# Performance work log

Hardware: AMD Instinct MI355X
Metric: run time of the kernel (lower is better)

Reference implementation:

```python
import jax, jax.numpy as jnp
import numpy as np

D_MODEL = 2048
N_Q_HEADS = 32
N_KV_HEADS = 8
HEAD_DIM = D_MODEL // N_Q_HEADS  # 64
KV_DIM = HEAD_DIM * N_KV_HEADS   # 512
B, S = 2, 2048


def setup_inputs() -> dict:
    key = jax.random.key(0)
    ks = jax.random.split(key, 11)
    sc_d = 1.0 / np.sqrt(D_MODEL)
    return {
        "query": jax.random.normal(ks[0], (B, S, D_MODEL), jnp.float32),
        "key":   jax.random.normal(ks[1], (B, S, D_MODEL), jnp.float32),
        "value": jax.random.normal(ks[2], (B, S, D_MODEL), jnp.float32),
        "Wq": jax.random.normal(ks[3], (D_MODEL, D_MODEL), jnp.float32) * sc_d,
        "bq": jnp.zeros((D_MODEL,), jnp.float32),
        "Wk": jax.random.normal(ks[4], (D_MODEL, KV_DIM), jnp.float32) * sc_d,
        "bk": jnp.zeros((KV_DIM,), jnp.float32),
        "Wv": jax.random.normal(ks[5], (D_MODEL, KV_DIM), jnp.float32) * sc_d,
        "bv": jnp.zeros((KV_DIM,), jnp.float32),
        "Wo": jax.random.normal(ks[6], (D_MODEL, D_MODEL), jnp.float32) * sc_d,
        "bo": jnp.zeros((D_MODEL,), jnp.float32),
    }


def reference(query, key, value, Wq, bq, Wk, bk, Wv, bv, Wo, bo):
    b, s, _ = query.shape
    g = N_Q_HEADS // N_KV_HEADS  # num groups
    # projections
    Q = query @ Wq + bq                      # [b, s, d_model]
    K = key @ Wk + bk                        # [b, s, kv_dim]
    V = value @ Wv + bv                      # [b, s, kv_dim]
    # split heads. Torch code splits Q into groups of num_kv_heads heads,
    # and each group broadcasts per-head against the Hkv KV heads, i.e.
    # query head (grp*Hkv + j) attends against kv head j.
    Q = Q.reshape(b, s, g, N_KV_HEADS, HEAD_DIM)  # [b, s, g, hkv, d]
    K = K.reshape(b, s, N_KV_HEADS, HEAD_DIM)     # [b, s, hkv, d]
    V = V.reshape(b, s, N_KV_HEADS, HEAD_DIM)
    scale = 1.0 / jnp.sqrt(jnp.float32(HEAD_DIM))
    scores = jnp.einsum('bsghd,bthd->bghst', Q, K) * scale  # [b,g,hkv,s,s]
    attn = jax.nn.softmax(scores, axis=-1)
    out = jnp.einsum('bghst,bthd->bsghd', attn, V)          # [b,s,g,hkv,d]
    # concat over groups then heads == original head order (g major, hkv minor)
    out = out.reshape(b, s, D_MODEL)
    return out @ Wo + bo
```

## Files before the change

kernel.cpp:

```cpp
#include <hip/hip_runtime.h>
#include <cstdint>

typedef _Float16 half4 __attribute__((ext_vector_type(4)));
typedef _Float16 half8 __attribute__((ext_vector_type(8)));
typedef _Float16 half16 __attribute__((ext_vector_type(16)));
typedef float f32x4 __attribute__((ext_vector_type(4)));
typedef float f32x16 __attribute__((ext_vector_type(16)));

#define L2E 1.44269504088896340736f

__device__ __forceinline__ void gl16(const void* g, void* l) {
  __builtin_amdgcn_global_load_lds(
      (const __attribute__((address_space(1))) void*)g,
      (__attribute__((address_space(3))) void*)l, 16, 0, 0);
}

__device__ __forceinline__ uint32_t pk2(float a, float b) {
  return __builtin_bit_cast(uint32_t, __builtin_amdgcn_cvt_pkrtz(a, b));
}

__device__ __forceinline__ void plswap(uint32_t& x, uint32_t& y) {
  auto r = __builtin_amdgcn_permlane32_swap((int)x, (int)y, false, false);
  x = (uint32_t)r[0];
  y = (uint32_t)r[1];
}

__device__ __forceinline__ f32x16 zero16() {
  f32x16 z;
  #pragma unroll
  for (int r = 0; r < 16; ++r) z[r] = 0.0f;
  return z;
}

__global__ __launch_bounds__(256) void cvt_f32_f16_3(
    const float* __restrict__ s0, const float* __restrict__ s1, const float* __restrict__ s2,
    _Float16* __restrict__ d0, _Float16* __restrict__ d1, _Float16* __restrict__ d2)
{
  const float* src = (blockIdx.z == 0) ? s0 : (blockIdx.z == 1 ? s1 : s2);
  _Float16* dst    = (blockIdx.z == 0) ? d0 : (blockIdx.z == 1 ? d1 : d2);
  size_t i = ((size_t)blockIdx.x * 256 + threadIdx.x) * 8;
  float4 a = *(const float4*)(src + i);
  float4 b = *(const float4*)(src + i + 4);
  half8 o;
  o[0] = (_Float16)a.x; o[1] = (_Float16)a.y; o[2] = (_Float16)a.z; o[3] = (_Float16)a.w;
  o[4] = (_Float16)b.x; o[5] = (_Float16)b.y; o[6] = (_Float16)b.z; o[7] = (_Float16)b.w;
  *(half8*)(dst + i) = o;
}

__global__ __launch_bounds__(256) void transpose_w_all(
    const float* __restrict__ Wq, const float* __restrict__ Wk,
    const float* __restrict__ Wv, const float* __restrict__ Wo,
    _Float16* __restrict__ WqkvT, _Float16* __restrict__ WoT)
{
  int id = blockIdx.x;
  const float* src;
  _Float16* dst;
  int N, tx, ty;
  if (id < 4096)      { src = Wq; dst = WqkvT;                        N = 2048; tx = id & 63; ty = id >> 6; }
  else if (id < 5120) { id -= 4096; src = Wk; dst = WqkvT + (size_t)2048 * 2048; N = 512; tx = id & 15; ty = id >> 4; }
  else if (id < 6144) { id -= 5120; src = Wv; dst = WqkvT + (size_t)2560 * 2048; N = 512; tx = id & 15; ty = id >> 4; }
  else                { id -= 6144; src = Wo; dst = WoT;              N = 2048; tx = id & 63; ty = id >> 6; }
  const int n0 = tx * 32, k0 = ty * 32;
  __shared__ float t[32][33];
  #pragma unroll
  for (int i = 0; i < 4; ++i)
    t[threadIdx.y + i * 8][threadIdx.x] =
        src[(size_t)(k0 + threadIdx.y + i * 8) * N + n0 + threadIdx.x];
  __syncthreads();
  #pragma unroll
  for (int i = 0; i < 4; ++i)
    dst[(size_t)(n0 + threadIdx.y + i * 8) * 2048 + k0 + threadIdx.x] =
        (_Float16)t[threadIdx.x][threadIdx.y + i * 8];
}

__global__ __launch_bounds__(256) void transpose_v(
    const _Float16* __restrict__ QKV, _Float16* __restrict__ VT)
{
  const int bh = blockIdx.z;
  const int bb = bh >> 3, h = bh & 7;
  const int t0 = blockIdx.x * 32, d0 = blockIdx.y * 32;
  __shared__ _Float16 t[32][33];
  const _Float16* src = QKV + (size_t)(bb * 2048) * 3072 + 2560 + h * 64;
  #pragma unroll
  for (int i = 0; i < 4; ++i)
    t[threadIdx.y + i * 8][threadIdx.x] =
        src[(size_t)(t0 + threadIdx.y + i * 8) * 3072 + d0 + threadIdx.x];
  __syncthreads();
  _Float16* dst = VT + ((size_t)(bb * 8 + h) * 64) * 2048;
  #pragma unroll
  for (int i = 0; i < 4; ++i)
    dst[(size_t)(d0 + threadIdx.y + i * 8) * 2048 + t0 + threadIdx.x] =
        t[threadIdx.x][threadIdx.y + i * 8];
}

template<int MODE>
__global__ __launch_bounds__(512, 2) void gemm128(
    const _Float16* __restrict__ Aq, const _Float16* __restrict__ Ak, const _Float16* __restrict__ Av,
    const _Float16* __restrict__ Bt,
    const float* __restrict__ bias0, const float* __restrict__ bias1, const float* __restrict__ bias2,
    _Float16* __restrict__ Ch, float* __restrict__ Cf)
{
  constexpr int K = 2048;
  constexpr int N = (MODE == 0) ? 3072 : 2048;
  constexpr int NB = N / 256;
  constexpr int G = 32 * NB;
  constexpr int BUF = 8192 + 16384;

  const int wg = blockIdx.x;
  const int work = (wg & 7) * (G / 8) + (wg >> 3);
  const int m0 = (work / NB) * 128;
  const int n0 = (work % NB) * 256;

  const _Float16* A = Aq;
  if constexpr (MODE == 0) { if (n0 >= 2560) A = Av; else if (n0 >= 2048) A = Ak; }

  const int tid = threadIdx.x;
  const int lane = tid & 63;
  const int w = tid >> 6;
  const int wr = w >> 2;
  const int wc = w & 3;
  const int lo = lane & 15, hi = lane >> 4;

  __shared__ __align__(1024) char smem[3 * BUF];

  f32x4 acc[4][4];
  #pragma unroll
  for (int mt = 0; mt < 4; ++mt)
    #pragma unroll
    for (int nt = 0; nt < 4; ++nt)
      acc[mt][nt] = (f32x4){0.f, 0.f, 0.f, 0.f};

  const _Float16* pB = Bt + (size_t)(n0 + w * 32 + (lane >> 2)) * K + (lane & 3) * 8;
  const _Float16* pA = A  + (size_t)(m0 + w * 16 + (lane >> 2)) * K + (lane & 3) * 8;
  const size_t bstep = (size_t)16 * K;
  const int dstB = 8192 + w * 2048;
  const int dstA = w * 1024;

  gl16(pA,      smem + dstA);
  gl16(pB,      smem + dstB);        gl16(pB + bstep,      smem + dstB + 1024);
  gl16(pA + 32, smem + BUF + dstA);
  gl16(pB + 32, smem + BUF + dstB);  gl16(pB + 32 + bstep, smem + BUF + dstB + 1024);
  pA += 64; pB += 64;
  asm volatile("s_waitcnt vmcnt(3)" ::: "memory");
  __builtin_amdgcn_s_barrier();

  const int abase = (wr * 64 + lo) * 64 + hi * 16;
  const int bbase = 8192 + (wc * 64 + lo) * 64 + hi * 16;

  int c = 0;
  for (int t = 0; t < 64; ++t) {
    int c1 = c + 1; if (c1 == 3) c1 = 0;
    int c2 = c1 + 1; if (c2 == 3) c2 = 0;
    if (t < 62) {
      char* bp_ = smem + c2 * BUF;
      gl16(pA, bp_ + dstA);
      gl16(pB, bp_ + dstB);
      gl16(pB + bstep, bp_ + dstB + 1024);
      pA += 32; pB += 32;
    }

    const char* bc = smem + c * BUF;
    half8 af[4], bf[4];
    #pragma unroll
    for (int mt = 0; mt < 4; ++mt) af[mt] = *(const half8*)(bc + abase + mt * 1024);
    #pragma unroll
    for (int nt = 0; nt < 4; ++nt) bf[nt] = *(const half8*)(bc + bbase + nt * 1024);

    __builtin_amdgcn_s_setprio(1);
    #pragma unroll
    for (int mt = 0; mt < 4; ++mt)
      #pragma unroll
      for (int nt = 0; nt < 4; ++nt)
        acc[mt][nt] = __builtin_amdgcn_mfma_f32_16x16x32_f16(af[mt], bf[nt], acc[mt][nt], 0, 0, 0);
    __builtin_amdgcn_s_setprio(0);

    if (t < 62)       asm volatile("s_waitcnt vmcnt(3)" ::: "memory");
    else if (t == 62) asm volatile("s_waitcnt vmcnt(0)" ::: "memory");
    if (t < 63) __builtin_amdgcn_s_barrier();
    c = c1;
  }

  float* T = (float*)smem;
  const int tr = tid >> 4;
  const int sc = tid & 15;
  #pragma unroll
  for (int mp = 0; mp < 4; ++mp) {
    __syncthreads();
    #pragma unroll
    for (int nt = 0; nt < 4; ++nt)
      #pragma unroll
      for (int r = 0; r < 4; ++r)
        T[(wr * 16 + 4 * hi + r) * 256 + wc * 64 + nt * 16 + lo] = acc[mp][nt][r];
    __syncthreads();
    const int grow = m0 + (tr >> 4) * 64 + mp * 16 + (tr & 15);
    const int gcol = n0 + sc * 16;
    const float* Trow = T + tr * 256 + sc * 16;
    float4 v[4];
    #pragma unroll
    for (int q = 0; q < 4; ++q) v[q] = ((const float4*)Trow)[q];
    const float* bp = bias0;
    int cb = gcol;
    if constexpr (MODE == 0) {
      if (gcol >= 2560) { bp = bias2; cb = gcol - 2560; }
      else if (gcol >= 2048) { bp = bias1; cb = gcol - 2048; }
    }
    float4 bvv[4];
    #pragma unroll
    for (int q = 0; q < 4; ++q) bvv[q] = ((const float4*)(bp + cb))[q];
    if constexpr (MODE == 0) {
      half16 o;
      #pragma unroll
      for (int q = 0; q < 4; ++q) {
        o[4 * q + 0] = (_Float16)(v[q].x + bvv[q].x);
        o[4 * q + 1] = (_Float16)(v[q].y + bvv[q].y);
        o[4 * q + 2] = (_Float16)(v[q].z + bvv[q].z);
        o[4 * q + 3] = (_Float16)(v[q].w + bvv[q].w);
      }
      *(half16*)(Ch + (size_t)grow * N + gcol) = o;
    } else {
      float* dstp = Cf + (size_t)grow * N + gcol;
      #pragma unroll
      for (int q = 0; q < 4; ++q) {
        float4 ov = {v[q].x + bvv[q].x, v[q].y + bvv[q].y, v[q].z + bvv[q].z, v[q].w + bvv[q].w};
        ((float4*)dstp)[q] = ov;
      }
    }
  }
}

__global__ __launch_bounds__(256, 5) void attn_fwd4(
    const _Float16* __restrict__ QKV, const _Float16* __restrict__ VT,
    _Float16* __restrict__ AO)
{
  const int wg = blockIdx.x;
  const int work = (wg & 7) * 128 + (wg >> 3);
  const int bh = work >> 6;
  const int b = bh >> 3, h = bh & 7;
  const int rem = work & 63;
  const int qh = (rem >> 4) * 8 + h;
  const int qt = rem & 15;

  const int tid = threadIdx.x;
  const int lane = tid & 63;
  const int w = tid >> 6;
  const int l31 = lane & 31;
  const int hi5 = lane >> 5;
  const int r7 = l31 & 7;

  __shared__ __align__(1024) char sm[2][2][8192];

  const _Float16 QSC = (_Float16)(0.125f * L2E);
  const int qrow0 = b * 2048 + qt * 128 + w * 32 + l31;
  half8 qf[4];
  {
    const _Float16* qp = QKV + (size_t)qrow0 * 3072 + qh * 64 + hi5 * 8;
    #pragma unroll
    for (int s = 0; s < 4; ++s) {
      half8 q = *(const half8*)(qp + s * 16);
      #pragma unroll
      for (int e = 0; e < 8; ++e) q[e] = q[e] * QSC;
      qf[s] = q;
    }
  }

  const int li = lane >> 3;
  const int lc = lane & 7;
  const int kslot = lc ^ li;
  const int w16li = w * 16 + li;
  const _Float16* Ksrc = QKV + ((size_t)(b * 2048 + w16li)) * 3072 + 2048 + h * 64 + kslot * 8;
  const _Float16* Vsrc = VT + ((size_t)(b * 8 + h) * 64 + w16li) * 2048 + kslot * 8;

  f32x16 oa[2];
  oa[0] = zero16();
  oa[1] = zero16();
  float lreg = 0.f;

  {
    char* kd = &sm[0][0][0] + w * 2048;
    char* vd = &sm[0][1][0] + w * 2048;
    gl16(Ksrc, kd);
    gl16(Ksrc + (size_t)8 * 3072, kd + 1024);
    gl16(Vsrc, vd);
    gl16(Vsrc + (size_t)8 * 2048, vd + 1024);
  }
  __syncthreads();

  int cur = 0;
  for (int t = 0; t < 32; ++t) {
    if (t < 31) {
      const int t0 = (t + 1) * 64;
      char* kd = &sm[cur ^ 1][0][0] + w * 2048;
      char* vd = &sm[cur ^ 1][1][0] + w * 2048;
      const _Float16* kg = Ksrc + (size_t)t0 * 3072;
      const _Float16* vg = Vsrc + t0;
      gl16(kg, kd);
      gl16(kg + (size_t)8 * 3072, kd + 1024);
      gl16(vg, vd);
      gl16(vg + (size_t)8 * 2048, vd + 1024);
    }

    const char* Kb = &sm[cur][0][0];
    const char* Vb = &sm[cur][1][0];

    uint32_t pw[4][4];
    float ps = 0.f;
    #pragma unroll
    for (int j = 0; j < 2; ++j) {
      f32x16 sa = zero16();
      const int kr = j * 32 + l31;
      __builtin_amdgcn_s_setprio(1);
      #pragma unroll
      for (int s = 0; s < 4; ++s) {
        half8 kf = *(const half8*)(Kb + kr * 128 + (((2 * s + hi5) ^ r7) << 4));
        sa = __builtin_amdgcn_mfma_f32_32x32x16_f16(kf, qf[s], sa, 0, 0, 0);
      }
      __builtin_amdgcn_s_setprio(0);
      #pragma unroll
      for (int r = 0; r < 16; ++r) {
        const float p = __builtin_amdgcn_exp2f(sa[r]);
        sa[r] = p;
        ps += p;
      }
      #pragma unroll
      for (int hf = 0; hf < 2; ++hf) {
        const int rb = hf * 8;
        uint32_t w0 = pk2(sa[rb + 0], sa[rb + 1]);
        uint32_t w1 = pk2(sa[rb + 2], sa[rb + 3]);
        uint32_t w2 = pk2(sa[rb + 4], sa[rb + 5]);
        uint32_t w3 = pk2(sa[rb + 6], sa[rb + 7]);
        plswap(w0, w2);
        plswap(w1, w3);
        const int s = 2 * j + hf;
        pw[s][0] = w0; pw[s][1] = w1; pw[s][2] = w2; pw[s][3] = w3;
      }
    }
    ps += __shfl_xor(ps, 32);
    lreg += ps;

    __builtin_amdgcn_s_setprio(1);
    #pragma unroll
    for (int s = 0; s < 4; ++s) {
      union { uint32_t u[4]; half8 h; } p0;
      #pragma unroll
      for (int u = 0; u < 4; ++u) p0.u[u] = pw[s][u];
      #pragma unroll
      for (int i = 0; i < 2; ++i) {
        const int vr = i * 32 + l31;
        half8 vf = *(const half8*)(Vb + vr * 128 + (((2 * s + hi5) ^ r7) << 4));
        oa[i] = __builtin_amdgcn_mfma_f32_32x32x16_f16(vf, p0.h, oa[i], 0, 0, 0);
      }
    }
    __builtin_amdgcn_s_setprio(0);

    __syncthreads();
    cur ^= 1;
  }

  {
    const float inv = 1.0f / lreg;
    #pragma unroll
    for (int i = 0; i < 2; ++i) {
      _Float16* dst = AO + (size_t)qrow0 * 2048 + qh * 64 + i * 32 + hi5 * 4;
      #pragma unroll
      for (int q = 0; q < 4; ++q) {
        union { uint32_t u[2]; half4 h4; } o;
        o.u[0] = pk2(oa[i][4 * q + 0] * inv, oa[i][4 * q + 1] * inv);
        o.u[1] = pk2(oa[i][4 * q + 2] * inv, oa[i][4 * q + 3] * inv);
        *(half4*)(dst + 8 * q) = o.h4;
      }
    }
  }
}

extern "C" void kernel_launch(void* const* d_in, const int* in_sizes, int n_in,
                              void* d_out, int out_size, void* d_ws, size_t ws_size,
                              hipStream_t stream) {
  const float* query = (const float*)d_in[0];
  const float* key   = (const float*)d_in[1];
  const float* value = (const float*)d_in[2];
  const float* Wq = (const float*)d_in[3];
  const float* bq = (const float*)d_in[4];
  const float* Wk = (const float*)d_in[5];
  const float* bk = (const float*)d_in[6];
  const float* Wv = (const float*)d_in[7];
  const float* bv = (const float*)d_in[8];
  const float* Wo = (const float*)d_in[9];
  const float* bo = (const float*)d_in[10];
  float* out = (float*)d_out;

  char* ws = (char*)d_ws;
  _Float16* qh    = (_Float16*)(ws);
  _Float16* kh    = (_Float16*)(ws + 16777216);
  _Float16* vh    = (_Float16*)(ws + 33554432);
  _Float16* WqkvT = (_Float16*)(ws + 50331648);
  _Float16* WoT   = (_Float16*)(ws + 62914560);
  _Float16* QKVh  = (_Float16*)(ws + 71303168);
  _Float16* VT    = (_Float16*)(ws + 96468992);
  _Float16* aoh   = (_Float16*)(ws + 100663296);

  cvt_f32_f16_3<<<dim3(4096, 1, 3), 256, 0, stream>>>(query, key, value, qh, kh, vh);
  transpose_w_all<<<10240, dim3(32, 8), 0, stream>>>(Wq, Wk, Wv, Wo, WqkvT, WoT);
  gemm128<0><<<384, 512, 0, stream>>>(qh, kh, vh, WqkvT, bq, bk, bv, QKVh, nullptr);
  transpose_v<<<dim3(64, 2, 16), dim3(32, 8), 0, stream>>>(QKVh, VT);
  attn_fwd4<<<1024, 256, 0, stream>>>(QKVh, VT, aoh);
  gemm128<1><<<256, 512, 0, stream>>>(aoh, nullptr, nullptr, WoT, bo,
                                      nullptr, nullptr, nullptr, out);
}
```

Measured before the change: 248.2 us.

## Triple-buffer attention K/V loads and merge prep kernels into one launch

The attention kernel moves from double to triple buffering of K/V tiles in LDS. It prefetches two tiles ahead and replaces the full __syncthreads with an explicit vmcnt wait plus barrier, so global loads overlap more compute. The occupancy hint drops from 5 to 3 blocks per CU to fit the larger LDS footprint. Separately, the f32-to-f16 input conversion and the weight transposes are fused into a single prep kernel launch, removing one launch.

Result: no change. 244.0 us (-1.7%).

```diff
diff --git a/kernel.cpp b/kernel.cpp
--- a/kernel.cpp
+++ b/kernel.cpp
@@ -32,27 +32,30 @@
   return z;
 }
 
-__global__ __launch_bounds__(256) void cvt_f32_f16_3(
-    const float* __restrict__ s0, const float* __restrict__ s1, const float* __restrict__ s2,
-    _Float16* __restrict__ d0, _Float16* __restrict__ d1, _Float16* __restrict__ d2)
-{
-  const float* src = (blockIdx.z == 0) ? s0 : (blockIdx.z == 1 ? s1 : s2);
-  _Float16* dst    = (blockIdx.z == 0) ? d0 : (blockIdx.z == 1 ? d1 : d2);
-  size_t i = ((size_t)blockIdx.x * 256 + threadIdx.x) * 8;
-  float4 a = *(const float4*)(src + i);
-  float4 b = *(const float4*)(src + i + 4);
-  half8 o;
-  o[0] = (_Float16)a.x; o[1] = (_Float16)a.y; o[2] = (_Float16)a.z; o[3] = (_Float16)a.w;
-  o[4] = (_Float16)b.x; o[5] = (_Float16)b.y; o[6] = (_Float16)b.z; o[7] = (_Float16)b.w;
-  *(half8*)(dst + i) = o;
-}
-
-__global__ __launch_bounds__(256) void transpose_w_all(
+__global__ __launch_bounds__(256) void prep_all(
+    const float* __restrict__ q, const float* __restrict__ k, const float* __restrict__ v,
     const float* __restrict__ Wq, const float* __restrict__ Wk,
     const float* __restrict__ Wv, const float* __restrict__ Wo,
+    _Float16* __restrict__ qh, _Float16* __restrict__ kh, _Float16* __restrict__ vh,
     _Float16* __restrict__ WqkvT, _Float16* __restrict__ WoT)
 {
   int id = blockIdx.x;
+  const int tid = threadIdx.y * 32 + threadIdx.x;
+  if (id < 12288) {
+    const int z = id >> 12;
+    const int x = id & 4095;
+    const float* src = (z == 0) ? q : (z == 1 ? k : v);
+    _Float16* dst    = (z == 0) ? qh : (z == 1 ? kh : vh);
+    size_t i = ((size_t)x * 256 + tid) * 8;
+    float4 a = *(const float4*)(src + i);
+    float4 b = *(const float4*)(src + i + 4);
+    half8 o;
+    o[0] = (_Float16)a.x; o[1] = (_Float16)a.y; o[2] = (_Float16)a.z; o[3] = (_Float16)a.w;
+    o[4] = (_Float16)b.x; o[5] = (_Float16)b.y; o[6] = (_Float16)b.z; o[7] = (_Float16)b.w;
+    *(half8*)(dst + i) = o;
+    return;
+  }
+  id -= 12288;
   const float* src;
   _Float16* dst;
   int N, tx, ty;
@@ -197,7 +200,7 @@
     const float* Trow = T + tr * 256 + sc * 16;
     float4 v[4];
     #pragma unroll
-    for (int q = 0; q < 4; ++q) v[q] = ((const float4*)Trow)[q];
+    for (int qq = 0; qq < 4; ++qq) v[qq] = ((const float4*)Trow)[qq];
     const float* bp = bias0;
     int cb = gcol;
     if constexpr (MODE == 0) {
@@ -206,29 +209,29 @@
     }
     float4 bvv[4];
     #pragma unroll
-    for (int q = 0; q < 4; ++q) bvv[q] = ((const float4*)(bp + cb))[q];
+    for (int qq = 0; qq < 4; ++qq) bvv[qq] = ((const float4*)(bp + cb))[qq];
     if constexpr (MODE == 0) {
       half16 o;
       #pragma unroll
-      for (int q = 0; q < 4; ++q) {
-        o[4 * q + 0] = (_Float16)(v[q].x + bvv[q].x);
-        o[4 * q + 1] = (_Float16)(v[q].y + bvv[q].y);
-        o[4 * q + 2] = (_Float16)(v[q].z + bvv[q].z);
-        o[4 * q + 3] = (_Float16)(v[q].w + bvv[q].w);
+      for (int qq = 0; qq < 4; ++qq) {
+        o[4 * qq + 0] = (_Float16)(v[qq].x + bvv[qq].x);
+        o[4 * qq + 1] = (_Float16)(v[qq].y + bvv[qq].y);
+        o[4 * qq + 2] = (_Float16)(v[qq].z + bvv[qq].z);
+        o[4 * qq + 3] = (_Float16)(v[qq].w + bvv[qq].w);
       }
       *(half16*)(Ch + (size_t)grow * N + gcol) = o;
     } else {
       float* dstp = Cf + (size_t)grow * N + gcol;
       #pragma unroll
-      for (int q = 0; q < 4; ++q) {
-        float4 ov = {v[q].x + bvv[q].x, v[q].y + bvv[q].y, v[q].z + bvv[q].z, v[q].w + bvv[q].w};
-        ((float4*)dstp)[q] = ov;
-      }
-    }
-  }
-}
-
-__global__ __launch_bounds__(256, 5) void attn_fwd4(
+      for (int qq = 0; qq < 4; ++qq) {
+        float4 ov = {v[qq].x + bvv[qq].x, v[qq].y + bvv[qq].y, v[qq].z + bvv[qq].z, v[qq].w + bvv[qq].w};
+        ((float4*)dstp)[qq] = ov;
+      }
+    }
+  }
+}
+
+__global__ __launch_bounds__(256, 3) void attn_fwd5(
     const _Float16* __restrict__ QKV, const _Float16* __restrict__ VT,
     _Float16* __restrict__ AO)
 {
@@ -247,7 +250,7 @@
   const int hi5 = lane >> 5;
   const int r7 = l31 & 7;
 
-  __shared__ __align__(1024) char sm[2][2][8192];
+  __shared__ __align__(1024) char sm[3][2][8192];
 
   const _Float16 QSC = (_Float16)(0.125f * L2E);
   const int qrow0 = b * 2048 + qt * 128 + w * 32 + l31;
@@ -275,29 +278,28 @@
   oa[1] = zero16();
   float lreg = 0.f;
 
-  {
-    char* kd = &sm[0][0][0] + w * 2048;
-    char* vd = &sm[0][1][0] + w * 2048;
-    gl16(Ksrc, kd);
-    gl16(Ksrc + (size_t)8 * 3072, kd + 1024);
-    gl16(Vsrc, vd);
-    gl16(Vsrc + (size_t)8 * 2048, vd + 1024);
-  }
-  __syncthreads();
+  #define STAGE_KV(buf, tile)                                                 \
+    do {                                                                      \
+      char* kd_ = &sm[(buf)][0][0] + w * 2048;                                \
+      char* vd_ = &sm[(buf)][1][0] + w * 2048;                                \
+      const _Float16* kg_ = Ksrc + (size_t)(tile) * 64 * 3072;                \
+      const _Float16* vg_ = Vsrc + (tile) * 64;                               \
+      gl16(kg_, kd_);                                                         \
+      gl16(kg_ + (size_t)8 * 3072, kd_ + 1024);                               \
+      gl16(vg_, vd_);                                                         \
+      gl16(vg_ + (size_t)8 * 2048, vd_ + 1024);                               \
+    } while (0)
+
+  STAGE_KV(0, 0);
+  STAGE_KV(1, 1);
+  asm volatile("s_waitcnt vmcnt(4)" ::: "memory");
+  __builtin_amdgcn_s_barrier();
 
   int cur = 0;
   for (int t = 0; t < 32; ++t) {
-    if (t < 31) {
-      const int t0 = (t + 1) * 64;
-      char* kd = &sm[cur ^ 1][0][0] + w * 2048;
-      char* vd = &sm[cur ^ 1][1][0] + w * 2048;
-      const _Float16* kg = Ksrc + (size_t)t0 * 3072;
-      const _Float16* vg = Vsrc + t0;
-      gl16(kg, kd);
-      gl16(kg + (size_t)8 * 3072, kd + 1024);
-      gl16(vg, vd);
-      gl16(vg + (size_t)8 * 2048, vd + 1024);
-    }
+    int c1 = cur + 1; if (c1 == 3) c1 = 0;
+    int c2 = c1 + 1; if (c2 == 3) c2 = 0;
+    if (t < 30) STAGE_KV(c2, t + 2);
 
     const char* Kb = &sm[cur][0][0];
     const char* Vb = &sm[cur][1][0];
@@ -352,9 +354,12 @@
     }
     __builtin_amdgcn_s_setprio(0);
 
-    __syncthreads();
-    cur ^= 1;
-  }
+    if (t < 30)       asm volatile("s_waitcnt vmcnt(4)" ::: "memory");
+    else if (t == 30) asm volatile("s_waitcnt vmcnt(0)" ::: "memory");
+    if (t < 31) __builtin_amdgcn_s_barrier();
+    cur = c1;
+  }
+  #undef STAGE_KV
 
   {
     const float inv = 1.0f / lreg;
@@ -398,11 +403,11 @@
   _Float16* VT    = (_Float16*)(ws + 96468992);
   _Float16* aoh   = (_Float16*)(ws + 100663296);
 
-  cvt_f32_f16_3<<<dim3(4096, 1, 3), 256, 0, stream>>>(query, key, value, qh, kh, vh);
-  transpose_w_all<<<10240, dim3(32, 8), 0, stream>>>(Wq, Wk, Wv, Wo, WqkvT, WoT);
+  prep_all<<<22528, dim3(32, 8), 0, stream>>>(query, key, value, Wq, Wk, Wv, Wo,
+                                              qh, kh, vh, WqkvT, WoT);
   gemm128<0><<<384, 512, 0, stream>>>(qh, kh, vh, WqkvT, bq, bk, bv, QKVh, nullptr);
   transpose_v<<<dim3(64, 2, 16), dim3(32, 8), 0, stream>>>(QKVh, VT);
-  attn_fwd4<<<1024, 256, 0, stream>>>(QKVh, VT, aoh);
+  attn_fwd5<<<1024, 256, 0, stream>>>(QKVh, VT, aoh);
   gemm128<1><<<256, 512, 0, stream>>>(aoh, nullptr, nullptr, WoT, bo,
                                       nullptr, nullptr, nullptr, out);
 }
```

## Merge prep kernels, halve QKV GEMM tile width, adjust attention occupancy

Applied to the files above, without the earlier changes.

Fuses the input f32->f16 conversion and the weight transpose kernels into one launch. The QKV projection GEMM now uses 128-wide N tiles instead of 256, which doubles the workgroup count from 384 to 768 so more CUs stay busy, at the cost of less B-operand reuse per tile. The attention kernel's launch bounds drop its occupancy hint from 5 to 4 waves, which may give it more registers per thread.

Result: faster. 239.2 us (-3.6%).

```diff
diff --git a/kernel.cpp b/kernel.cpp
--- a/kernel.cpp
+++ b/kernel.cpp
@@ -32,27 +32,30 @@
   return z;
 }
 
-__global__ __launch_bounds__(256) void cvt_f32_f16_3(
-    const float* __restrict__ s0, const float* __restrict__ s1, const float* __restrict__ s2,
-    _Float16* __restrict__ d0, _Float16* __restrict__ d1, _Float16* __restrict__ d2)
-{
-  const float* src = (blockIdx.z == 0) ? s0 : (blockIdx.z == 1 ? s1 : s2);
-  _Float16* dst    = (blockIdx.z == 0) ? d0 : (blockIdx.z == 1 ? d1 : d2);
-  size_t i = ((size_t)blockIdx.x * 256 + threadIdx.x) * 8;
-  float4 a = *(const float4*)(src + i);
-  float4 b = *(const float4*)(src + i + 4);
-  half8 o;
-  o[0] = (_Float16)a.x; o[1] = (_Float16)a.y; o[2] = (_Float16)a.z; o[3] = (_Float16)a.w;
-  o[4] = (_Float16)b.x; o[5] = (_Float16)b.y; o[6] = (_Float16)b.z; o[7] = (_Float16)b.w;
-  *(half8*)(dst + i) = o;
-}
-
-__global__ __launch_bounds__(256) void transpose_w_all(
+__global__ __launch_bounds__(256) void prep_all(
+    const float* __restrict__ q, const float* __restrict__ k, const float* __restrict__ v,
     const float* __restrict__ Wq, const float* __restrict__ Wk,
     const float* __restrict__ Wv, const float* __restrict__ Wo,
+    _Float16* __restrict__ qh, _Float16* __restrict__ kh, _Float16* __restrict__ vh,
     _Float16* __restrict__ WqkvT, _Float16* __restrict__ WoT)
 {
   int id = blockIdx.x;
+  const int tid = threadIdx.y * 32 + threadIdx.x;
+  if (id < 12288) {
+    const int z = id >> 12;
+    const int x = id & 4095;
+    const float* src = (z == 0) ? q : (z == 1 ? k : v);
+    _Float16* dst    = (z == 0) ? qh : (z == 1 ? kh : vh);
+    size_t i = ((size_t)x * 256 + tid) * 8;
+    float4 a = *(const float4*)(src + i);
+    float4 b = *(const float4*)(src + i + 4);
+    half8 o;
+    o[0] = (_Float16)a.x; o[1] = (_Float16)a.y; o[2] = (_Float16)a.z; o[3] = (_Float16)a.w;
+    o[4] = (_Float16)b.x; o[5] = (_Float16)b.y; o[6] = (_Float16)b.z; o[7] = (_Float16)b.w;
+    *(half8*)(dst + i) = o;
+    return;
+  }
+  id -= 12288;
   const float* src;
   _Float16* dst;
   int N, tx, ty;
@@ -102,14 +105,18 @@
 {
   constexpr int K = 2048;
   constexpr int N = (MODE == 0) ? 3072 : 2048;
-  constexpr int NB = N / 256;
+  constexpr int BN = (MODE == 0) ? 128 : 256;
+  constexpr int NB = N / BN;
   constexpr int G = 32 * NB;
-  constexpr int BUF = 8192 + 16384;
+  constexpr int BUFB = BN * 64;
+  constexpr int BUF = 8192 + BUFB;
+  constexpr int NT = BN / 64;
+  constexpr int NVM = 1 + BN / 128;
 
   const int wg = blockIdx.x;
   const int work = (wg & 7) * (G / 8) + (wg >> 3);
   const int m0 = (work / NB) * 128;
-  const int n0 = (work % NB) * 256;
+  const int n0 = (work % NB) * BN;
 
   const _Float16* A = Aq;
   if constexpr (MODE == 0) { if (n0 >= 2560) A = Av; else if (n0 >= 2048) A = Ak; }
@@ -123,112 +130,118 @@
 
   __shared__ __align__(1024) char smem[3 * BUF];
 
-  f32x4 acc[4][4];
+  f32x4 acc[4][NT];
   #pragma unroll
   for (int mt = 0; mt < 4; ++mt)
     #pragma unroll
-    for (int nt = 0; nt < 4; ++nt)
+    for (int nt = 0; nt < NT; ++nt)
       acc[mt][nt] = (f32x4){0.f, 0.f, 0.f, 0.f};
 
-  const _Float16* pB = Bt + (size_t)(n0 + w * 32 + (lane >> 2)) * K + (lane & 3) * 8;
+  const _Float16* pB = Bt + (size_t)(n0 + w * (BN / 8) + (lane >> 2)) * K + (lane & 3) * 8;
   const _Float16* pA = A  + (size_t)(m0 + w * 16 + (lane >> 2)) * K + (lane & 3) * 8;
   const size_t bstep = (size_t)16 * K;
-  const int dstB = 8192 + w * 2048;
+  const int dstB = 8192 + w * (BN / 8) * 64;
   const int dstA = w * 1024;
 
-  gl16(pA,      smem + dstA);
-  gl16(pB,      smem + dstB);        gl16(pB + bstep,      smem + dstB + 1024);
-  gl16(pA + 32, smem + BUF + dstA);
-  gl16(pB + 32, smem + BUF + dstB);  gl16(pB + 32 + bstep, smem + BUF + dstB + 1024);
-  pA += 64; pB += 64;
-  asm volatile("s_waitcnt vmcnt(3)" ::: "memory");
+  #define STAGE(base)                                                         \
+    do {                                                                      \
+      gl16(pA, (base) + dstA);                                                \
+      gl16(pB, (base) + dstB);                                                \
+      if constexpr (MODE == 1) gl16(pB + bstep, (base) + dstB + 1024);        \
+    } while (0)
+
+  STAGE(smem);
+  pA += 32; pB += 32;
+  STAGE(smem + BUF);
+  pA += 32; pB += 32;
+  asm volatile("s_waitcnt vmcnt(%0)" :: "i"(NVM) : "memory");
   __builtin_amdgcn_s_barrier();
 
   const int abase = (wr * 64 + lo) * 64 + hi * 16;
-  const int bbase = 8192 + (wc * 64 + lo) * 64 + hi * 16;
+  const int bbase = 8192 + (wc * (BN / 4) + lo) * 64 + hi * 16;
 
   int c = 0;
   for (int t = 0; t < 64; ++t) {
     int c1 = c + 1; if (c1 == 3) c1 = 0;
     int c2 = c1 + 1; if (c2 == 3) c2 = 0;
     if (t < 62) {
-      char* bp_ = smem + c2 * BUF;
-      gl16(pA, bp_ + dstA);
-      gl16(pB, bp_ + dstB);
-      gl16(pB + bstep, bp_ + dstB + 1024);
+      STAGE(smem + c2 * BUF);
       pA += 32; pB += 32;
     }
 
     const char* bc = smem + c * BUF;
-    half8 af[4], bf[4];
+    half8 af[4], bf[NT];
     #pragma unroll
     for (int mt = 0; mt < 4; ++mt) af[mt] = *(const half8*)(bc + abase + mt * 1024);
     #pragma unroll
-    for (int nt = 0; nt < 4; ++nt) bf[nt] = *(const half8*)(bc + bbase + nt * 1024);
+    for (int nt = 0; nt < NT; ++nt) bf[nt] = *(const half8*)(bc + bbase + nt * 1024);
 
     __builtin_amdgcn_s_setprio(1);
     #pragma unroll
     for (int mt = 0; mt < 4; ++mt)
       #pragma unroll
-      for (int nt = 0; nt < 4; ++nt)
+      for (int nt = 0; nt < NT; ++nt)
         acc[mt][nt] = __builtin_amdgcn_mfma_f32_16x16x32_f16(af[mt], bf[nt], acc[mt][nt], 0, 0, 0);
     __builtin_amdgcn_s_setprio(0);
 
-    if (t < 62)       asm volatile("s_waitcnt vmcnt(3)" ::: "memory");
+    if (t < 62)       asm volatile("s_waitcnt vmcnt(%0)" :: "i"(NVM) : "memory");
     else if (t == 62) asm volatile("s_waitcnt vmcnt(0)" ::: "memory");
     if (t < 63) __builtin_amdgcn_s_barrier();
     c = c1;
   }
+  #undef STAGE
 
   float* T = (float*)smem;
   const int tr = tid >> 4;
   const int sc = tid & 15;
+  constexpr int CPS = BN / 16;
   #pragma unroll
   for (int mp = 0; mp < 4; ++mp) {
     __syncthreads();
     #pragma unroll
-    for (int nt = 0; nt < 4; ++nt)
+    for (int nt = 0; nt < NT; ++nt)
       #pragma unroll
       for (int r = 0; r < 4; ++r)
-        T[(wr * 16 + 4 * hi + r) * 256 + wc * 64 + nt * 16 + lo] = acc[mp][nt][r];
+        T[(wr * 16 + 4 * hi + r) * BN + wc * (BN / 4) + nt * 16 + lo] = acc[mp][nt][r];
     __syncthreads();
     const int grow = m0 + (tr >> 4) * 64 + mp * 16 + (tr & 15);
-    const int gcol = n0 + sc * 16;
-    const float* Trow = T + tr * 256 + sc * 16;
-    float4 v[4];
-    #pragma unroll
-    for (int q = 0; q < 4; ++q) v[q] = ((const float4*)Trow)[q];
+    const int gcol = n0 + sc * CPS;
+    const float* Trow = T + tr * BN + sc * CPS;
     const float* bp = bias0;
     int cb = gcol;
     if constexpr (MODE == 0) {
       if (gcol >= 2560) { bp = bias2; cb = gcol - 2560; }
       else if (gcol >= 2048) { bp = bias1; cb = gcol - 2048; }
     }
-    float4 bvv[4];
-    #pragma unroll
-    for (int q = 0; q < 4; ++q) bvv[q] = ((const float4*)(bp + cb))[q];
     if constexpr (MODE == 0) {
-      half16 o;
-      #pragma unroll
-      for (int q = 0; q < 4; ++q) {
-        o[4 * q + 0] = (_Float16)(v[q].x + bvv[q].x);
-        o[4 * q + 1] = (_Float16)(v[q].y + bvv[q].y);
-        o[4 * q + 2] = (_Float16)(v[q].z + bvv[q].z);
-        o[4 * q + 3] = (_Float16)(v[q].w + bvv[q].w);
-      }
-      *(half16*)(Ch + (size_t)grow * N + gcol) = o;
+      float4 v0 = ((const float4*)Trow)[0];
+      float4 v1 = ((const float4*)Trow)[1];
+      float4 b0 = ((const float4*)(bp + cb))[0];
+      float4 b1 = ((const float4*)(bp + cb))[1];
+      half8 o;
+      o[0] = (_Float16)(v0.x + b0.x); o[1] = (_Float16)(v0.y + b0.y);
+      o[2] = (_Float16)(v0.z + b0.z); o[3] = (_Float16)(v0.w + b0.w);
+      o[4] = (_Float16)(v1.x + b1.x); o[5] = (_Float16)(v1.y + b1.y);
+      o[6] = (_Float16)(v1.z + b1.z); o[7] = (_Float16)(v1.w + b1.w);
+      *(half8*)(Ch + (size_t)grow * N + gcol) = o;
     } else {
+      float4 v[4];
+      #pragma unroll
+      for (int qq = 0; qq < 4; ++qq) v[qq] = ((const float4*)Trow)[qq];
+      float4 bvv[4];
+      #pragma unroll
+      for (int qq = 0; qq < 4; ++qq) bvv[qq] = ((const float4*)(bp + cb))[qq];
       float* dstp = Cf + (size_t)grow * N + gcol;
       #pragma unroll
-      for (int q = 0; q < 4; ++q) {
-        float4 ov = {v[q].x + bvv[q].x, v[q].y + bvv[q].y, v[q].z + bvv[q].z, v[q].w + bvv[q].w};
-        ((float4*)dstp)[q] = ov;
-      }
-    }
-  }
-}
-
-__global__ __launch_bounds__(256, 5) void attn_fwd4(
+      for (int qq = 0; qq < 4; ++qq) {
+        float4 ov = {v[qq].x + bvv[qq].x, v[qq].y + bvv[qq].y, v[qq].z + bvv[qq].z, v[qq].w + bvv[qq].w};
+        ((float4*)dstp)[qq] = ov;
+      }
+    }
+  }
+}
+
+__global__ __launch_bounds__(256, 4) void attn_fwd4(
     const _Float16* __restrict__ QKV, const _Float16* __restrict__ VT,
     _Float16* __restrict__ AO)
 {
@@ -398,9 +411,9 @@
   _Float16* VT    = (_Float16*)(ws + 96468992);
   _Float16* aoh   = (_Float16*)(ws + 100663296);
 
-  cvt_f32_f16_3<<<dim3(4096, 1, 3), 256, 0, stream>>>(query, key, value, qh, kh, vh);
-  transpose_w_all<<<10240, dim3(32, 8), 0, stream>>>(Wq, Wk, Wv, Wo, WqkvT, WoT);
-  gemm128<0><<<384, 512, 0, stream>>>(qh, kh, vh, WqkvT, bq, bk, bv, QKVh, nullptr);
+  prep_all<<<22528, dim3(32, 8), 0, stream>>>(query, key, value, Wq, Wk, Wv, Wo,
+                                              qh, kh, vh, WqkvT, WoT);
+  gemm128<0><<<768, 512, 0, stream>>>(qh, kh, vh, WqkvT, bq, bk, bv, QKVh, nullptr);
   transpose_v<<<dim3(64, 2, 16), dim3(32, 8), 0, stream>>>(QKVh, VT);
   attn_fwd4<<<1024, 256, 0, stream>>>(QKVh, VT, aoh);
   gemm128<1><<<256, 512, 0, stream>>>(aoh, nullptr, nullptr, WoT, bo,
```
